# Performance work log

Measured on AMD Instinct MI355X. Metric: run time of the kernel, lower is better.

## Reference

```python
import jax, jax.numpy as jnp
import numpy as np

G = 1024      # graphs per batch
NPG = 64      # nodes per graph
M = 512       # undirected edges per graph (stored both directions)
N = G * NPG   # 65536 nodes
E = G * 2 * M # 1048576 directed edges
F_IN = 128
HID = 128
CLS = 10
RATIO = 0.5   # top-k edge ratio (forward arg `ratio`); eval phase (train_phase=False)


def setup_inputs() -> dict:
    rng = np.random.default_rng(0)
    # random undirected edges within each graph, i < j guaranteed
    a = rng.integers(0, NPG, (G, M))
    b = rng.integers(0, NPG - 1, (G, M))
    b = b + (b >= a)  # b != a
    i = np.minimum(a, b)
    j = np.maximum(a, b)
    off = (np.arange(G) * NPG)[:, None]
    src = (np.concatenate([i, j], axis=1) + off).reshape(-1).astype(np.int32)
    dst = (np.concatenate([j, i], axis=1) + off).reshape(-1).astype(np.int32)
    # reverse-edge pairing: within each graph block of 2M edges, fwd e <-> e+M
    rev = (np.concatenate([np.arange(M) + M, np.arange(M)])[None, :]
           + (np.arange(G) * 2 * M)[:, None]).reshape(-1).astype(np.int32)
    batch = np.repeat(np.arange(G), NPG).astype(np.int32)

    key = jax.random.key(0)
    ks = jax.random.split(key, 8)

    def lin(k, fi, fo):
        return jax.random.normal(k, (fi, fo), jnp.float32) / np.sqrt(fi).astype(np.float32)

    return dict(
        x=jax.random.normal(ks[0], (N, F_IN), jnp.float32),
        src=jnp.asarray(src), dst=jnp.asarray(dst), rev=jnp.asarray(rev),
        batch=jnp.asarray(batch),
        W0=lin(ks[1], F_IN, HID), b0=jnp.zeros((HID,), jnp.float32),
        W1=lin(ks[2], HID, HID), b1=jnp.zeros((HID,), jnp.float32),
        W2=lin(ks[3], HID, HID), b2=jnp.zeros((HID,), jnp.float32),
        lw1=lin(ks[4], HID, HID), lb1=jnp.zeros((HID,), jnp.float32),
        lw2=lin(ks[5], HID, CLS), lb2=jnp.zeros((CLS,), jnp.float32),
    )


def gcn_conv(x, W, b, src, dst, ew):
    # PyG GCNConv with self-loops (fill 1) and symmetric normalization
    h = x @ W                                      # [N,H]
    deg = jax.ops.segment_sum(ew, dst, num_segments=N) + 1.0
    dinv = jax.lax.rsqrt(deg)                      # deg >= 1 (relu'd x => ew >= 0)
    norm = dinv[src] * ew * dinv[dst]              # [E]
    agg = jax.ops.segment_sum(norm[:, None] * h[src], dst, num_segments=N)
    return agg + (dinv * dinv)[:, None] * h + b    # self-loop term + bias


def reference(x, src, dst, rev, batch, W0, b0, W1, b1, W2, b2, lw1, lb1, lw2, lb2):
    ones_e = jnp.ones((E,), x.dtype)
    x1 = jax.nn.relu(gcn_conv(x, W0, b0, src, dst, ones_e))

    # edge scores on relu'd features (nonnegative)
    scores = jnp.sum(x1[src] * x1[dst], axis=-1)   # [E]
    gid = batch[src]                               # per-edge graph id (nondecreasing)
    mask = src < dst                               # one direction per undirected edge

    # per-graph (segment) top-k over masked edges: rank within segment by score desc
    smask = jnp.where(mask, scores, -jnp.inf)
    perm = jnp.lexsort((-smask, gid))              # primary: gid, secondary: score desc
    counts = jax.ops.segment_sum(jnp.ones((E,), jnp.int32), gid, num_segments=G)
    start = jnp.cumsum(counts) - counts            # exclusive segment starts
    rank = jnp.zeros((E,), jnp.int32).at[perm].set(
        jnp.arange(E, dtype=jnp.int32) - start[gid[perm]])
    m = jax.ops.segment_sum(mask.astype(jnp.int32), gid, num_segments=G)
    k = jnp.ceil(RATIO * m.astype(jnp.float32)).astype(jnp.int32)
    sel = mask & (rank < k[gid])
    sampled = (sel | sel[rev]).astype(x.dtype)     # mirror to reverse direction

    ew = scores * sampled                          # sparse edge weights
    x2 = jax.nn.relu(gcn_conv(x1, W1, b1, src, dst, ew))
    x3 = jax.nn.relu(gcn_conv(x2, W2, b2, src, dst, ew))

    # global mean pool over nodes per graph
    nc = jax.ops.segment_sum(jnp.ones((N,), x.dtype), batch, num_segments=G)
    pooled = jax.ops.segment_sum(x3, batch, num_segments=G) / nc[:, None]

    h = jax.nn.relu(pooled @ lw1 + lb1)            # dropout is identity at eval
    logits = h @ lw2 + lb2
    return (jax.nn.log_softmax(logits, axis=-1), sampled, counts)
```

## Files before the change

### kernel.cpp

```cpp
#include <hip/hip_runtime.h>

#define G_   1024
#define NPG_ 64
#define EPG_ 1024
#define MPG_ 512
#define F_   128
#define E_   (G_*EPG_)

typedef __attribute__((ext_vector_type(8))) short bf16x8;
typedef __attribute__((ext_vector_type(4))) float f32x4;

__device__ __forceinline__ unsigned short f2bf(float f) {
    union { float f; unsigned int u; } v; v.f = f;
    unsigned int r = v.u + 0x7fffu + ((v.u >> 16) & 1u);
    return (unsigned short)(r >> 16);
}
__device__ __forceinline__ unsigned int packbf(float a, float b) {
    return (unsigned int)f2bf(a) | ((unsigned int)f2bf(b) << 16);
}

#define XASW(r, cb) ((((r) << 4) + ((cb) ^ ((r) & 15))) << 3)
#define AFSW(r, b)  ((((r) << 3) + ((b) ^ ((r) & 7))) << 3)

__global__ __launch_bounds__(256) void k_pack_w(const float* __restrict__ W0,
    const float* __restrict__ W1, const float* __restrict__ W2,
    unsigned short* __restrict__ Wp)
{
    int idx = blockIdx.x * 256 + threadIdx.x;
    int wsel = idx >> 11;
    int r = idx & 2047;
    int lane = r & 63, tc = (r >> 6) & 7, kb = r >> 9;
    const float* W = (wsel == 0) ? W0 : ((wsel == 1) ? W1 : W2);
    int col  = tc * 16 + (lane & 15);
    int row0 = kb * 32 + (lane >> 4) * 8;
    unsigned int p0 = packbf(W[(row0+0)*F_+col], W[(row0+1)*F_+col]);
    unsigned int p1 = packbf(W[(row0+2)*F_+col], W[(row0+3)*F_+col]);
    unsigned int p2 = packbf(W[(row0+4)*F_+col], W[(row0+5)*F_+col]);
    unsigned int p3 = packbf(W[(row0+6)*F_+col], W[(row0+7)*F_+col]);
    *(uint4*)(Wp + (size_t)wsel * 16384 + (size_t)r * 8) = make_uint4(p0,p1,p2,p3);
}

__global__ __launch_bounds__(256, 4) void k_fused(
    const float* __restrict__ x, const int* __restrict__ src, const int* __restrict__ dst,
    const unsigned short* __restrict__ Wp,
    const float* __restrict__ b0, const float* __restrict__ b1, const float* __restrict__ b2,
    const float* __restrict__ lw1, const float* __restrict__ lb1,
    const float* __restrict__ lw2, const float* __restrict__ lb2,
    float* __restrict__ out_log, float* __restrict__ out_sampled,
    float* __restrict__ out_counts)
{
    const int g = blockIdx.x, t = threadIdx.x;
    const int l = t & 63, w = t >> 6;
    const int q = l >> 4, cl = l & 15;
    const int base_e = g * EPG_, base_n = g * NPG_;

    __shared__ alignas(16) unsigned short XA[8192];
    __shared__ alignas(16) float buf1[4224];
    __shared__ alignas(16) float sc[MPG_];
    __shared__ unsigned char sl[EPG_], dl[EPG_];
    __shared__ int hist_i[256];
    __shared__ unsigned long long mlist[96];
    __shared__ int wsum[4];
    __shared__ float redzf[8];
    __shared__ int ideg[NPG_];
    __shared__ float dinv[NPG_];
    __shared__ int mcnt, bstar, Rrem;

    float* mtmp = (float*)hist_i;
    unsigned int*   a1p = (unsigned int*)buf1;
    unsigned short* af1 = (unsigned short*)buf1 + 4224;
    unsigned short* af2 = (unsigned short*)buf1;

    auto mfma_step1 = [&](const unsigned short* WpX, f32x4 (&cX)[4][2]) {
        #pragma unroll
        for (int rb = 0; rb < 4; rb++) { cX[rb][0] = (f32x4)0.0f; cX[rb][1] = (f32x4)0.0f; }
        #pragma unroll
        for (int kb = 0; kb < 4; kb++) {
            bf16x8 a[4];
            #pragma unroll
            for (int rb = 0; rb < 4; rb++)
                a[rb] = *(const bf16x8*)&XA[XASW(rb*16 + cl, kb*4 + q)];
            #pragma unroll
            for (int tcw = 0; tcw < 2; tcw++) {
                bf16x8 b = *(const bf16x8*)&WpX[((kb*8 + 2*w+tcw)*64 + l)*8];
                #pragma unroll
                for (int rb = 0; rb < 4; rb++)
                    cX[rb][tcw] = __builtin_amdgcn_mfma_f32_16x16x32_bf16(
                                      a[rb], b, cX[rb][tcw], 0, 0, 0);
            }
        }
    };
    auto write_xw = [&](const f32x4 (&cX)[4][2]) {
        #pragma unroll
        for (int rb = 0; rb < 4; rb++)
            #pragma unroll
            for (int tcw = 0; tcw < 2; tcw++) {
                int tc = 2*w + tcw;
                #pragma unroll
                for (int rp = 0; rp < 2; rp++) {
                    int r0 = rb*16 + q*4 + rp*2;
                    int idx = ((r0 >> 5)*8 + tc)*512 + (((r0 >> 3) & 3)*16 + cl)*8 + (r0 & 7);
                    *(unsigned int*)&XA[idx] = packbf(cX[rb][tcw][rp*2], cX[rb][tcw][rp*2+1]);
                }
            }
    };
    auto mfma_step2 = [&](const unsigned short* AFp, f32x4 (&cX)[4][2]) {
        #pragma unroll
        for (int rb = 0; rb < 4; rb++) { cX[rb][0] = (f32x4)0.0f; cX[rb][1] = (f32x4)0.0f; }
        #pragma unroll
        for (int kb2 = 0; kb2 < 2; kb2++) {
            bf16x8 a2[4];
            #pragma unroll
            for (int rb = 0; rb < 4; rb++)
                a2[rb] = *(const bf16x8*)&AFp[AFSW(rb*16 + cl, kb2*4 + q)];
            #pragma unroll
            for (int tcw = 0; tcw < 2; tcw++) {
                bf16x8 b2 = *(const bf16x8*)&XA[((kb2*8 + 2*w+tcw)*64 + l)*8];
                #pragma unroll
                for (int rb = 0; rb < 4; rb++)
                    cX[rb][tcw] = __builtin_amdgcn_mfma_f32_16x16x32_bf16(
                                      a2[rb], b2, cX[rb][tcw], 0, 0, 0);
            }
        }
    };
    auto epilogue_H = [&](const f32x4 (&cX)[4][2], const float* bias) {
        #pragma unroll
        for (int tcw = 0; tcw < 2; tcw++) {
            int colb = (2*w + tcw)*16 + cl;
            float bv = bias[colb];
            #pragma unroll
            for (int rb = 0; rb < 4; rb++)
                #pragma unroll
                for (int reg = 0; reg < 4; reg++) {
                    int row = rb*16 + q*4 + reg;
                    XA[XASW(row, colb >> 3) + (colb & 7)] =
                        f2bf(fmaxf(cX[rb][tcw][reg] + bv, 0.0f));
                }
        }
    };

    const float4* xsrc = (const float4*)(x + (size_t)base_n * F_);
    for (int i = t; i < 2048; i += 256) {
        int v = i >> 5, c4 = i & 31;
        float4 xv = xsrc[i];
        int si = XASW(v, c4 >> 1) + (c4 & 1) * 4;
        unsigned int* d2 = (unsigned int*)&XA[si];
        d2[0] = packbf(xv.x, xv.y);
        d2[1] = packbf(xv.z, xv.w);
    }
    for (int i = t; i < 2112; i += 256) a1p[i] = 0u;
    if (t < NPG_) ideg[t] = 0;
    __syncthreads();

    {
        int4 s4 = ((const int4*)(src + base_e))[t];
        int4 d4 = ((const int4*)(dst + base_e))[t];
        int s0 = s4.x - base_n, s1 = s4.y - base_n, s2 = s4.z - base_n, s3 = s4.w - base_n;
        int d0 = d4.x - base_n, d1 = d4.y - base_n, d2 = d4.z - base_n, d3 = d4.w - base_n;
        *(uchar4*)&sl[t*4] = make_uchar4((unsigned char)s0, (unsigned char)s1,
                                         (unsigned char)s2, (unsigned char)s3);
        *(uchar4*)&dl[t*4] = make_uchar4((unsigned char)d0, (unsigned char)d1,
                                         (unsigned char)d2, (unsigned char)d3);
        atomicAdd(&ideg[d0], 1); atomicAdd(&ideg[d1], 1);
        atomicAdd(&ideg[d2], 1); atomicAdd(&ideg[d3], 1);
        atomicAdd(&a1p[d0 * 33 + (s0 >> 1)], 1u << ((s0 & 1) * 16));
        atomicAdd(&a1p[d1 * 33 + (s1 >> 1)], 1u << ((s1 & 1) * 16));
        atomicAdd(&a1p[d2 * 33 + (s2 >> 1)], 1u << ((s2 & 1) * 16));
        atomicAdd(&a1p[d3 * 33 + (s3 >> 1)], 1u << ((s3 & 1) * 16));
    }
    __syncthreads();

    {
        f32x4 cA[4][2];
        mfma_step1(Wp, cA);
        for (int i = t; i < 4096; i += 256) {
            int v = i >> 6, s = i & 63;
            unsigned int m = (a1p[v * 33 + (s >> 1)] >> ((s & 1) * 16)) & 0xFFFFu;
            float fv = rsqrtf((float)(ideg[v] + 1)), fs = rsqrtf((float)(ideg[s] + 1));
            float a = fv * fs * (float)m;
            if (v == s) a += fv * fv;
            af1[AFSW(v, s >> 3) + (s & 7)] = f2bf(a);
        }
        __syncthreads();
        write_xw(cA);
    }
    __syncthreads();

    {
        f32x4 cB[4][2];
        mfma_step2(af1, cB);
        __syncthreads();
        epilogue_H(cB, b0);
    }
    __syncthreads();

    {
        f32x4 cg[4];
        #pragma unroll
        for (int tcg = 0; tcg < 4; tcg++) cg[tcg] = (f32x4)0.0f;
        #pragma unroll
        for (int kb = 0; kb < 4; kb++) {
            bf16x8 a_g = *(const bf16x8*)&XA[XASW(w*16 + cl, kb*4 + q)];
            #pragma unroll
            for (int tcg = 0; tcg < 4; tcg++) {
                bf16x8 b = *(const bf16x8*)&XA[XASW(tcg*16 + cl, kb*4 + q)];
                cg[tcg] = __builtin_amdgcn_mfma_f32_16x16x32_bf16(a_g, b, cg[tcg], 0, 0, 0);
            }
        }
        #pragma unroll
        for (int tcg = 0; tcg < 4; tcg++)
            #pragma unroll
            for (int reg = 0; reg < 4; reg++)
                buf1[(w*16 + q*4 + reg)*66 + tcg*16 + cl] = cg[tcg][reg];
    }
    __syncthreads();

    float sA, sB;
    {
        f32x4 cC[4][2];
        mfma_step1(Wp + 16384, cC);
        sA = buf1[(int)sl[t]*66 + dl[t]];
        sB = buf1[(int)sl[t+256]*66 + dl[t+256]];
        sc[t] = sA; sc[t + 256] = sB;
        __syncthreads();
        write_xw(cC);
    }
    if (t < NPG_) dinv[t] = 1.0f;
    {
        float mn = fminf(sA, sB), mx = fmaxf(sA, sB);
        #pragma unroll
        for (int off = 32; off >= 1; off >>= 1) {
            mn = fminf(mn, __shfl_xor(mn, off, 64));
            mx = fmaxf(mx, __shfl_xor(mx, off, 64));
        }
        if (l == 0) { redzf[w] = mn; redzf[4 + w] = mx; }
    }
    hist_i[t] = 0;
    if (t == 0) mcnt = 0;
    __syncthreads();

    int selA, selB;
    {
        float mn = fminf(fminf(redzf[0], redzf[1]), fminf(redzf[2], redzf[3]));
        float mx = fmaxf(fmaxf(redzf[4], redzf[5]), fmaxf(redzf[6], redzf[7]));
        float scale = 255.0f / fmaxf(mx - mn, 1e-20f);
        int binA = (int)fminf((sA - mn) * scale, 255.0f);
        int binB = (int)fminf((sB - mn) * scale, 255.0f);
        atomicAdd(&hist_i[binA], 1);
        atomicAdd(&hist_i[binB], 1);
        for (int i = t; i < 4224; i += 256) buf1[i] = 0.0f;
        __syncthreads();
        int h = hist_i[t];
        int v = h;
        #pragma unroll
        for (int off = 1; off < 64; off <<= 1) {
            int n = __shfl_down(v, off, 64);
            if (l + off < 64) v += n;
        }
        if (l == 0) wsum[w] = v;
        __syncthreads();
        int suf = v;
        for (int w2 = w + 1; w2 < 4; w2++) suf += wsum[w2];
        int cgt = suf - h;
        if (suf >= 256 && cgt < 256) { bstar = t; Rrem = 256 - cgt; }
        __syncthreads();
        const int bs = bstar, Rr = Rrem;
        unsigned long long keyA = ((unsigned long long)__float_as_uint(sA) << 32)
                                | (unsigned int)(0xFFFFFFFFu - (unsigned)t);
        unsigned long long keyB = ((unsigned long long)__float_as_uint(sB) << 32)
                                | (unsigned int)(0xFFFFFFFFu - (unsigned)(t + 256));
        if (binA == bs) { int p = atomicAdd(&mcnt, 1); if (p < 96) mlist[p] = keyA; }
        if (binB == bs) { int p = atomicAdd(&mcnt, 1); if (p < 96) mlist[p] = keyB; }
        __syncthreads();
        const int mc = mcnt;
        auto sel_edge = [&](float s, int e, int bin, unsigned long long key) -> int {
            if (bin > bs) return 1;
            if (bin < bs) return 0;
            if (mc <= 96) {
                int r = 0;
                for (int j2 = 0; j2 < mc; j2++) r += (mlist[j2] > key) ? 1 : 0;
                return r < Rr;
            }
            int r = 0;
            for (int ep = 0; ep < MPG_; ep++) {
                float sp = sc[ep];
                r += (sp > s || (sp == s && ep < e)) ? 1 : 0;
            }
            return r < 256;
        };
        selA = sel_edge(sA, t, binA, keyA);
        selB = sel_edge(sB, t + 256, binB, keyB);
        float sfA = selA ? 1.0f : 0.0f, sfB = selB ? 1.0f : 0.0f;
        out_sampled[base_e + t] = sfA;
        out_sampled[base_e + MPG_ + t] = sfA;
        out_sampled[base_e + t + 256] = sfB;
        out_sampled[base_e + MPG_ + t + 256] = sfB;
    }
    if (selA) {
        atomicAdd(&dinv[dl[t]], sA); atomicAdd(&dinv[sl[t]], sA);
        atomicAdd(&buf1[(int)dl[t]*66 + sl[t]], sA);
        atomicAdd(&buf1[(int)sl[t]*66 + dl[t]], sA);
    }
    if (selB) {
        atomicAdd(&dinv[dl[t+256]], sB); atomicAdd(&dinv[sl[t+256]], sB);
        atomicAdd(&buf1[(int)dl[t+256]*66 + sl[t+256]], sB);
        atomicAdd(&buf1[(int)sl[t+256]*66 + dl[t+256]], sB);
    }
    __syncthreads();
    if (t < NPG_) dinv[t] = rsqrtf(dinv[t]);
    if (t < F_)  sc[t] = 0.0f;
    __syncthreads();
    {
        float st[4];
        #pragma unroll
        for (int k2 = 0; k2 < 4; k2++) {
            int i = k2*256 + t; int vv = i >> 6, ss = i & 63;
            float a = dinv[vv] * dinv[ss] * buf1[vv*66 + ss];
            if (vv == ss) a += dinv[vv] * dinv[vv];
            st[k2] = a;
        }
        __syncthreads();
        #pragma unroll
        for (int k2 = 0; k2 < 4; k2++) {
            int i = k2*256 + t; int vv = i >> 6, ss = i & 63;
            af2[AFSW(vv, ss >> 3) + (ss & 7)] = f2bf(st[k2]);
        }
        for (int i = 1024 + t; i < 4096; i += 256) {
            int vv = i >> 6, ss = i & 63;
            float a = dinv[vv] * dinv[ss] * buf1[vv*66 + ss];
            if (vv == ss) a += dinv[vv] * dinv[vv];
            af2[AFSW(vv, ss >> 3) + (ss & 7)] = f2bf(a);
        }
    }
    __syncthreads();

    {
        f32x4 cB[4][2];
        mfma_step2(af2, cB);
        __syncthreads();
        epilogue_H(cB, b1);
    }
    __syncthreads();

    {
        f32x4 cA[4][2];
        mfma_step1(Wp + 32768, cA);
        __syncthreads();
        write_xw(cA);
        __syncthreads();
        f32x4 cB[4][2];
        mfma_step2(af2, cB);
        __syncthreads();
        #pragma unroll
        for (int tcw = 0; tcw < 2; tcw++) {
            int colb = (2*w + tcw)*16 + cl;
            float bv = b2[colb];
            float ps = 0.0f;
            #pragma unroll
            for (int rb = 0; rb < 4; rb++)
                #pragma unroll
                for (int reg = 0; reg < 4; reg++)
                    ps += fmaxf(cB[rb][tcw][reg] + bv, 0.0f);
            atomicAdd(&sc[colb], ps);
        }
    }
    __syncthreads();

    {
        int c = t & 127, hh = t >> 7;
        float p = 0.0f;
        for (int kk = 0; kk < 64; kk++) {
            int k2 = hh*64 + kk;
            p = fmaf(sc[k2], lw1[(size_t)k2 * F_ + c], p);
        }
        mtmp[t] = p;
    }
    __syncthreads();
    if (t >= 128 && t < 138) buf1[200 + (t - 128)] = 0.0f;
    if (t < F_)
        buf1[t] = fmaxf(lb1[t] + (mtmp[t] + mtmp[t + 128]) * (1.0f/64.0f), 0.0f);
    __syncthreads();
    if (t < 160) {
        int o = t >> 4, seg = t & 15;
        float p = 0.0f;
        #pragma unroll
        for (int kk = 0; kk < 8; kk++) {
            int k2 = seg*8 + kk;
            p = fmaf(buf1[k2], lw2[(size_t)k2 * 10 + o], p);
        }
        atomicAdd(&buf1[200 + o], p);
    }
    __syncthreads();
    if (t < 10) {
        float lg = buf1[200 + t] + lb2[t];
        float m = -1e30f;
        #pragma unroll
        for (int q2 = 0; q2 < 10; q2++) m = fmaxf(m, buf1[200 + q2] + lb2[q2]);
        float se = 0.0f;
        #pragma unroll
        for (int q2 = 0; q2 < 10; q2++) se += expf(buf1[200 + q2] + lb2[q2] - m);
        out_log[(size_t)g * 10 + t] = lg - m - logf(se);
    }
    if (t == 0) out_counts[g] = 1024.0f;
}

extern "C" void kernel_launch(void* const* d_in, const int* in_sizes, int n_in,
                              void* d_out, int out_size, void* d_ws, size_t ws_size,
                              hipStream_t stream) {
    const float* x    = (const float*)d_in[0];
    const int*   src  = (const int*)  d_in[1];
    const int*   dst  = (const int*)  d_in[2];
    const float* W0   = (const float*)d_in[5];
    const float* b0   = (const float*)d_in[6];
    const float* W1   = (const float*)d_in[7];
    const float* b1   = (const float*)d_in[8];
    const float* W2   = (const float*)d_in[9];
    const float* b2   = (const float*)d_in[10];
    const float* lw1  = (const float*)d_in[11];
    const float* lb1  = (const float*)d_in[12];
    const float* lw2  = (const float*)d_in[13];
    const float* lb2  = (const float*)d_in[14];

    float* out_log     = (float*)d_out;
    float* out_sampled = out_log + (size_t)G_ * 10;
    float* out_counts  = out_sampled + (size_t)E_;

    unsigned short* Wp = (unsigned short*)d_ws;

    k_pack_w<<<24, 256, 0, stream>>>(W0, W1, W2, Wp);
    k_fused<<<G_, 256, 0, stream>>>(x, src, dst, Wp, b0, b1, b2,
                                    lw1, lb1, lw2, lb2,
                                    out_log, out_sampled, out_counts);
}
```

Before: 48.34 us.

## Double block size to 512 threads, one column tile per wave

```diff
diff --git a/kernel.cpp b/kernel.cpp
--- a/kernel.cpp
+++ b/kernel.cpp
@@ -40,7 +40,7 @@
     *(uint4*)(Wp + (size_t)wsel * 16384 + (size_t)r * 8) = make_uint4(p0,p1,p2,p3);
 }
 
-__global__ __launch_bounds__(256, 4) void k_fused(
+__global__ __launch_bounds__(512, 8) void k_fused(
     const float* __restrict__ x, const int* __restrict__ src, const int* __restrict__ dst,
     const unsigned short* __restrict__ Wp,
     const float* __restrict__ b0, const float* __restrict__ b1, const float* __restrict__ b2,
@@ -61,86 +61,66 @@
     __shared__ int hist_i[256];
     __shared__ unsigned long long mlist[96];
     __shared__ int wsum[4];
-    __shared__ float redzf[8];
+    __shared__ float redzf[16];
     __shared__ int ideg[NPG_];
     __shared__ float dinv[NPG_];
     __shared__ int mcnt, bstar, Rrem;
 
-    float* mtmp = (float*)hist_i;
     unsigned int*   a1p = (unsigned int*)buf1;
     unsigned short* af1 = (unsigned short*)buf1 + 4224;
     unsigned short* af2 = (unsigned short*)buf1;
 
-    auto mfma_step1 = [&](const unsigned short* WpX, f32x4 (&cX)[4][2]) {
-        #pragma unroll
-        for (int rb = 0; rb < 4; rb++) { cX[rb][0] = (f32x4)0.0f; cX[rb][1] = (f32x4)0.0f; }
+    auto mfma_step1 = [&](const unsigned short* WpX, f32x4 (&cX)[4]) {
+        #pragma unroll
+        for (int rb = 0; rb < 4; rb++) cX[rb] = (f32x4)0.0f;
         #pragma unroll
         for (int kb = 0; kb < 4; kb++) {
-            bf16x8 a[4];
-            #pragma unroll
-            for (int rb = 0; rb < 4; rb++)
-                a[rb] = *(const bf16x8*)&XA[XASW(rb*16 + cl, kb*4 + q)];
-            #pragma unroll
-            for (int tcw = 0; tcw < 2; tcw++) {
-                bf16x8 b = *(const bf16x8*)&WpX[((kb*8 + 2*w+tcw)*64 + l)*8];
-                #pragma unroll
-                for (int rb = 0; rb < 4; rb++)
-                    cX[rb][tcw] = __builtin_amdgcn_mfma_f32_16x16x32_bf16(
-                                      a[rb], b, cX[rb][tcw], 0, 0, 0);
+            bf16x8 b = *(const bf16x8*)&WpX[((kb*8 + w)*64 + l)*8];
+            #pragma unroll
+            for (int rb = 0; rb < 4; rb++) {
+                bf16x8 a = *(const bf16x8*)&XA[XASW(rb*16 + cl, kb*4 + q)];
+                cX[rb] = __builtin_amdgcn_mfma_f32_16x16x32_bf16(a, b, cX[rb], 0, 0, 0);
             }
         }
     };
-    auto write_xw = [&](const f32x4 (&cX)[4][2]) {
+    auto write_xw = [&](const f32x4 (&cX)[4]) {
         #pragma unroll
         for (int rb = 0; rb < 4; rb++)
             #pragma unroll
-            for (int tcw = 0; tcw < 2; tcw++) {
-                int tc = 2*w + tcw;
-                #pragma unroll
-                for (int rp = 0; rp < 2; rp++) {
-                    int r0 = rb*16 + q*4 + rp*2;
-                    int idx = ((r0 >> 5)*8 + tc)*512 + (((r0 >> 3) & 3)*16 + cl)*8 + (r0 & 7);
-                    *(unsigned int*)&XA[idx] = packbf(cX[rb][tcw][rp*2], cX[rb][tcw][rp*2+1]);
-                }
+            for (int rp = 0; rp < 2; rp++) {
+                int r0 = rb*16 + q*4 + rp*2;
+                int idx = ((r0 >> 5)*8 + w)*512 + (((r0 >> 3) & 3)*16 + cl)*8 + (r0 & 7);
+                *(unsigned int*)&XA[idx] = packbf(cX[rb][rp*2], cX[rb][rp*2+1]);
             }
     };
-    auto mfma_step2 = [&](const unsigned short* AFp, f32x4 (&cX)[4][2]) {
-        #pragma unroll
-        for (int rb = 0; rb < 4; rb++) { cX[rb][0] = (f32x4)0.0f; cX[rb][1] = (f32x4)0.0f; }
+    auto mfma_step2 = [&](const unsigned short* AFp, f32x4 (&cX)[4]) {
+        #pragma unroll
+        for (int rb = 0; rb < 4; rb++) cX[rb] = (f32x4)0.0f;
         #pragma unroll
         for (int kb2 = 0; kb2 < 2; kb2++) {
-            bf16x8 a2[4];
-            #pragma unroll
-            for (int rb = 0; rb < 4; rb++)
-                a2[rb] = *(const bf16x8*)&AFp[AFSW(rb*16 + cl, kb2*4 + q)];
-            #pragma unroll
-            for (int tcw = 0; tcw < 2; tcw++) {
-                bf16x8 b2 = *(const bf16x8*)&XA[((kb2*8 + 2*w+tcw)*64 + l)*8];
-                #pragma unroll
-                for (int rb = 0; rb < 4; rb++)
-                    cX[rb][tcw] = __builtin_amdgcn_mfma_f32_16x16x32_bf16(
-                                      a2[rb], b2, cX[rb][tcw], 0, 0, 0);
+            bf16x8 b2 = *(const bf16x8*)&XA[((kb2*8 + w)*64 + l)*8];
+            #pragma unroll
+            for (int rb = 0; rb < 4; rb++) {
+                bf16x8 a2 = *(const bf16x8*)&AFp[AFSW(rb*16 + cl, kb2*4 + q)];
+                cX[rb] = __builtin_amdgcn_mfma_f32_16x16x32_bf16(a2, b2, cX[rb], 0, 0, 0);
             }
         }
     };
-    auto epilogue_H = [&](const f32x4 (&cX)[4][2], const float* bias) {
-        #pragma unroll
-        for (int tcw = 0; tcw < 2; tcw++) {
-            int colb = (2*w + tcw)*16 + cl;
-            float bv = bias[colb];
-            #pragma unroll
-            for (int rb = 0; rb < 4; rb++)
-                #pragma unroll
-                for (int reg = 0; reg < 4; reg++) {
-                    int row = rb*16 + q*4 + reg;
-                    XA[XASW(row, colb >> 3) + (colb & 7)] =
-                        f2bf(fmaxf(cX[rb][tcw][reg] + bv, 0.0f));
-                }
-        }
+    auto epilogue_H = [&](const f32x4 (&cX)[4], const float* bias) {
+        int colb = w*16 + cl;
+        float bv = bias[colb];
+        #pragma unroll
+        for (int rb = 0; rb < 4; rb++)
+            #pragma unroll
+            for (int reg = 0; reg < 4; reg++) {
+                int row = rb*16 + q*4 + reg;
+                XA[XASW(row, colb >> 3) + (colb & 7)] =
+                    f2bf(fmaxf(cX[rb][reg] + bv, 0.0f));
+            }
     };
 
     const float4* xsrc = (const float4*)(x + (size_t)base_n * F_);
-    for (int i = t; i < 2048; i += 256) {
+    for (int i = t; i < 2048; i += 512) {
         int v = i >> 5, c4 = i & 31;
         float4 xv = xsrc[i];
         int si = XASW(v, c4 >> 1) + (c4 & 1) * 4;
@@ -148,32 +128,27 @@
         d2[0] = packbf(xv.x, xv.y);
         d2[1] = packbf(xv.z, xv.w);
     }
-    for (int i = t; i < 2112; i += 256) a1p[i] = 0u;
+    for (int i = t; i < 2112; i += 512) a1p[i] = 0u;
     if (t < NPG_) ideg[t] = 0;
     __syncthreads();
 
     {
-        int4 s4 = ((const int4*)(src + base_e))[t];
-        int4 d4 = ((const int4*)(dst + base_e))[t];
-        int s0 = s4.x - base_n, s1 = s4.y - base_n, s2 = s4.z - base_n, s3 = s4.w - base_n;
-        int d0 = d4.x - base_n, d1 = d4.y - base_n, d2 = d4.z - base_n, d3 = d4.w - base_n;
-        *(uchar4*)&sl[t*4] = make_uchar4((unsigned char)s0, (unsigned char)s1,
-                                         (unsigned char)s2, (unsigned char)s3);
-        *(uchar4*)&dl[t*4] = make_uchar4((unsigned char)d0, (unsigned char)d1,
-                                         (unsigned char)d2, (unsigned char)d3);
+        int2 s2 = ((const int2*)(src + base_e))[t];
+        int2 d2 = ((const int2*)(dst + base_e))[t];
+        int s0 = s2.x - base_n, s1 = s2.y - base_n;
+        int d0 = d2.x - base_n, d1 = d2.y - base_n;
+        sl[t*2]   = (unsigned char)s0; sl[t*2+1] = (unsigned char)s1;
+        dl[t*2]   = (unsigned char)d0; dl[t*2+1] = (unsigned char)d1;
         atomicAdd(&ideg[d0], 1); atomicAdd(&ideg[d1], 1);
-        atomicAdd(&ideg[d2], 1); atomicAdd(&ideg[d3], 1);
         atomicAdd(&a1p[d0 * 33 + (s0 >> 1)], 1u << ((s0 & 1) * 16));
         atomicAdd(&a1p[d1 * 33 + (s1 >> 1)], 1u << ((s1 & 1) * 16));
-        atomicAdd(&a1p[d2 * 33 + (s2 >> 1)], 1u << ((s2 & 1) * 16));
-        atomicAdd(&a1p[d3 * 33 + (s3 >> 1)], 1u << ((s3 & 1) * 16));
-    }
-    __syncthreads();
-
-    {
-        f32x4 cA[4][2];
+    }
+    __syncthreads();
+
+    {
+        f32x4 cA[4];
         mfma_step1(Wp, cA);
-        for (int i = t; i < 4096; i += 256) {
+        for (int i = t; i < 4096; i += 512) {
             int v = i >> 6, s = i & 63;
             unsigned int m = (a1p[v * 33 + (s >> 1)] >> ((s & 1) * 16)) & 0xFFFFu;
             float fv = rsqrtf((float)(ideg[v] + 1)), fs = rsqrtf((float)(ideg[s] + 1));
@@ -187,7 +162,7 @@
     __syncthreads();
 
     {
-        f32x4 cB[4][2];
+        f32x4 cB[4];
         mfma_step2(af1, cB);
         __syncthreads();
         epilogue_H(cB, b0);
@@ -195,147 +170,131 @@
     __syncthreads();
 
     {
-        f32x4 cg[4];
-        #pragma unroll
-        for (int tcg = 0; tcg < 4; tcg++) cg[tcg] = (f32x4)0.0f;
+        const int rt = w & 3, ct0 = (w >> 2) * 2;
+        f32x4 cg[2];
+        cg[0] = (f32x4)0.0f; cg[1] = (f32x4)0.0f;
         #pragma unroll
         for (int kb = 0; kb < 4; kb++) {
-            bf16x8 a_g = *(const bf16x8*)&XA[XASW(w*16 + cl, kb*4 + q)];
-            #pragma unroll
-            for (int tcg = 0; tcg < 4; tcg++) {
-                bf16x8 b = *(const bf16x8*)&XA[XASW(tcg*16 + cl, kb*4 + q)];
-                cg[tcg] = __builtin_amdgcn_mfma_f32_16x16x32_bf16(a_g, b, cg[tcg], 0, 0, 0);
-            }
-        }
-        #pragma unroll
-        for (int tcg = 0; tcg < 4; tcg++)
+            bf16x8 a_g = *(const bf16x8*)&XA[XASW(rt*16 + cl, kb*4 + q)];
+            #pragma unroll
+            for (int j = 0; j < 2; j++) {
+                bf16x8 b = *(const bf16x8*)&XA[XASW((ct0+j)*16 + cl, kb*4 + q)];
+                cg[j] = __builtin_amdgcn_mfma_f32_16x16x32_bf16(a_g, b, cg[j], 0, 0, 0);
+            }
+        }
+        #pragma unroll
+        for (int j = 0; j < 2; j++)
             #pragma unroll
             for (int reg = 0; reg < 4; reg++)
-                buf1[(w*16 + q*4 + reg)*66 + tcg*16 + cl] = cg[tcg][reg];
-    }
-    __syncthreads();
-
-    float sA, sB;
-    {
-        f32x4 cC[4][2];
+                buf1[(rt*16 + q*4 + reg)*66 + (ct0+j)*16 + cl] = cg[j][reg];
+    }
+    __syncthreads();
+
+    float sA;
+    {
+        f32x4 cC[4];
         mfma_step1(Wp + 16384, cC);
         sA = buf1[(int)sl[t]*66 + dl[t]];
-        sB = buf1[(int)sl[t+256]*66 + dl[t+256]];
-        sc[t] = sA; sc[t + 256] = sB;
+        sc[t] = sA;
         __syncthreads();
         write_xw(cC);
     }
     if (t < NPG_) dinv[t] = 1.0f;
     {
-        float mn = fminf(sA, sB), mx = fmaxf(sA, sB);
+        float mn = sA, mx = sA;
         #pragma unroll
         for (int off = 32; off >= 1; off >>= 1) {
             mn = fminf(mn, __shfl_xor(mn, off, 64));
             mx = fmaxf(mx, __shfl_xor(mx, off, 64));
         }
-        if (l == 0) { redzf[w] = mn; redzf[4 + w] = mx; }
-    }
-    hist_i[t] = 0;
+        if (l == 0) { redzf[w] = mn; redzf[8 + w] = mx; }
+    }
+    if (t < 256) hist_i[t] = 0;
     if (t == 0) mcnt = 0;
     __syncthreads();
 
-    int selA, selB;
-    {
-        float mn = fminf(fminf(redzf[0], redzf[1]), fminf(redzf[2], redzf[3]));
-        float mx = fmaxf(fmaxf(redzf[4], redzf[5]), fmaxf(redzf[6], redzf[7]));
+    int selA;
+    {
+        float mn = redzf[0], mx = redzf[8];
+        #pragma unroll
+        for (int j = 1; j < 8; j++) { mn = fminf(mn, redzf[j]); mx = fmaxf(mx, redzf[8+j]); }
         float scale = 255.0f / fmaxf(mx - mn, 1e-20f);
         int binA = (int)fminf((sA - mn) * scale, 255.0f);
-        int binB = (int)fminf((sB - mn) * scale, 255.0f);
         atomicAdd(&hist_i[binA], 1);
-        atomicAdd(&hist_i[binB], 1);
-        for (int i = t; i < 4224; i += 256) buf1[i] = 0.0f;
-        __syncthreads();
-        int h = hist_i[t];
-        int v = h;
-        #pragma unroll
-        for (int off = 1; off < 64; off <<= 1) {
-            int n = __shfl_down(v, off, 64);
-            if (l + off < 64) v += n;
-        }
-        if (l == 0) wsum[w] = v;
-        __syncthreads();
-        int suf = v;
-        for (int w2 = w + 1; w2 < 4; w2++) suf += wsum[w2];
-        int cgt = suf - h;
-        if (suf >= 256 && cgt < 256) { bstar = t; Rrem = 256 - cgt; }
+        for (int i = t; i < 4224; i += 512) buf1[i] = 0.0f;
+        __syncthreads();
+        int h = 0, v = 0;
+        if (t < 256) {
+            h = hist_i[t];
+            v = h;
+            #pragma unroll
+            for (int off = 1; off < 64; off <<= 1) {
+                int n = __shfl_down(v, off, 64);
+                if (l + off < 64) v += n;
+            }
+            if (l == 0) wsum[w] = v;
+        }
+        __syncthreads();
+        if (t < 256) {
+            int suf = v;
+            for (int w2 = w + 1; w2 < 4; w2++) suf += wsum[w2];
+            int cgt = suf - h;
+            if (suf >= 256 && cgt < 256) { bstar = t; Rrem = 256 - cgt; }
+        }
         __syncthreads();
         const int bs = bstar, Rr = Rrem;
         unsigned long long keyA = ((unsigned long long)__float_as_uint(sA) << 32)
                                 | (unsigned int)(0xFFFFFFFFu - (unsigned)t);
-        unsigned long long keyB = ((unsigned long long)__float_as_uint(sB) << 32)
-                                | (unsigned int)(0xFFFFFFFFu - (unsigned)(t + 256));
         if (binA == bs) { int p = atomicAdd(&mcnt, 1); if (p < 96) mlist[p] = keyA; }
-        if (binB == bs) { int p = atomicAdd(&mcnt, 1); if (p < 96) mlist[p] = keyB; }
         __syncthreads();
         const int mc = mcnt;
-        auto sel_edge = [&](float s, int e, int bin, unsigned long long key) -> int {
-            if (bin > bs) return 1;
-            if (bin < bs) return 0;
-            if (mc <= 96) {
-                int r = 0;
-                for (int j2 = 0; j2 < mc; j2++) r += (mlist[j2] > key) ? 1 : 0;
-                return r < Rr;
-            }
+        if (binA > bs) selA = 1;
+        else if (binA < bs) selA = 0;
+        else if (mc <= 96) {
+            int r = 0;
+            for (int j2 = 0; j2 < mc; j2++) r += (mlist[j2] > keyA) ? 1 : 0;
+            selA = r < Rr;
+        } else {
             int r = 0;
             for (int ep = 0; ep < MPG_; ep++) {
                 float sp = sc[ep];
-                r += (sp > s || (sp == s && ep < e)) ? 1 : 0;
-            }
-            return r < 256;
-        };
-        selA = sel_edge(sA, t, binA, keyA);
-        selB = sel_edge(sB, t + 256, binB, keyB);
-        float sfA = selA ? 1.0f : 0.0f, sfB = selB ? 1.0f : 0.0f;
+                r += (sp > sA || (sp == sA && ep < t)) ? 1 : 0;
+            }
+            selA = r < 256;
+        }
+        float sfA = selA ? 1.0f : 0.0f;
         out_sampled[base_e + t] = sfA;
         out_sampled[base_e + MPG_ + t] = sfA;
-        out_sampled[base_e + t + 256] = sfB;
-        out_sampled[base_e + MPG_ + t + 256] = sfB;
     }
     if (selA) {
         atomicAdd(&dinv[dl[t]], sA); atomicAdd(&dinv[sl[t]], sA);
         atomicAdd(&buf1[(int)dl[t]*66 + sl[t]], sA);
         atomicAdd(&buf1[(int)sl[t]*66 + dl[t]], sA);
     }
-    if (selB) {
-        atomicAdd(&dinv[dl[t+256]], sB); atomicAdd(&dinv[sl[t+256]], sB);
-        atomicAdd(&buf1[(int)dl[t+256]*66 + sl[t+256]], sB);
-        atomicAdd(&buf1[(int)sl[t+256]*66 + dl[t+256]], sB);
-    }
     __syncthreads();
     if (t < NPG_) dinv[t] = rsqrtf(dinv[t]);
     if (t < F_)  sc[t] = 0.0f;
     __syncthreads();
     {
-        float st[4];
-        #pragma unroll
-        for (int k2 = 0; k2 < 4; k2++) {
-            int i = k2*256 + t; int vv = i >> 6, ss = i & 63;
+        float st[8];
+        #pragma unroll
+        for (int k2 = 0; k2 < 8; k2++) {
+            int i = k2*512 + t; int vv = i >> 6, ss = i & 63;
             float a = dinv[vv] * dinv[ss] * buf1[vv*66 + ss];
             if (vv == ss) a += dinv[vv] * dinv[vv];
             st[k2] = a;
         }
         __syncthreads();
         #pragma unroll
-        for (int k2 = 0; k2 < 4; k2++) {
-            int i = k2*256 + t; int vv = i >> 6, ss = i & 63;
+        for (int k2 = 0; k2 < 8; k2++) {
+            int i = k2*512 + t; int vv = i >> 6, ss = i & 63;
             af2[AFSW(vv, ss >> 3) + (ss & 7)] = f2bf(st[k2]);
         }
-        for (int i = 1024 + t; i < 4096; i += 256) {
-            int vv = i >> 6, ss = i & 63;
-            float a = dinv[vv] * dinv[ss] * buf1[vv*66 + ss];
-            if (vv == ss) a += dinv[vv] * dinv[vv];
-            af2[AFSW(vv, ss >> 3) + (ss & 7)] = f2bf(a);
-        }
-    }
-    __syncthreads();
-
-    {
-        f32x4 cB[4][2];
+    }
+    __syncthreads();
+
+    {
+        f32x4 cB[4];
         mfma_step2(af2, cB);
         __syncthreads();
         epilogue_H(cB, b1);
@@ -343,42 +302,40 @@
     __syncthreads();
 
     {
-        f32x4 cA[4][2];
+        f32x4 cA[4];
         mfma_step1(Wp + 32768, cA);
         __syncthreads();
         write_xw(cA);
         __syncthreads();
-        f32x4 cB[4][2];
+        f32x4 cB[4];
         mfma_step2(af2, cB);
         __syncthreads();
-        #pragma unroll
-        for (int tcw = 0; tcw < 2; tcw++) {
-            int colb = (2*w + tcw)*16 + cl;
-            float bv = b2[colb];
-            float ps = 0.0f;
-            #pragma unroll
-            for (int rb = 0; rb < 4; rb++)
-                #pragma unroll
-                for (int reg = 0; reg < 4; reg++)
-                    ps += fmaxf(cB[rb][tcw][reg] + bv, 0.0f);
-            atomicAdd(&sc[colb], ps);
-        }
+        int colb = w*16 + cl;
+        float bv = b2[colb];
+        float ps = 0.0f;
+        #pragma unroll
+        for (int rb = 0; rb < 4; rb++)
+            #pragma unroll
+            for (int reg = 0; reg < 4; reg++)
+                ps += fmaxf(cB[rb][reg] + bv, 0.0f);
+        atomicAdd(&sc[colb], ps);
+        if (t < 10) buf1[700 + t] = 0.0f;
     }
     __syncthreads();
 
     {
         int c = t & 127, hh = t >> 7;
         float p = 0.0f;
-        for (int kk = 0; kk < 64; kk++) {
-            int k2 = hh*64 + kk;
+        for (int kk = 0; kk < 32; kk++) {
+            int k2 = hh*32 + kk;
             p = fmaf(sc[k2], lw1[(size_t)k2 * F_ + c], p);
         }
-        mtmp[t] = p;
-    }
-    __syncthreads();
-    if (t >= 128 && t < 138) buf1[200 + (t - 128)] = 0.0f;
+        buf1[hh * 128 + c] = p;
+    }
+    __syncthreads();
     if (t < F_)
-        buf1[t] = fmaxf(lb1[t] + (mtmp[t] + mtmp[t + 128]) * (1.0f/64.0f), 0.0f);
+        buf1[512 + t] = fmaxf(lb1[t] + (buf1[t] + buf1[128+t] + buf1[256+t] + buf1[384+t])
+                                        * (1.0f/64.0f), 0.0f);
     __syncthreads();
     if (t < 160) {
         int o = t >> 4, seg = t & 15;
@@ -386,19 +343,19 @@
         #pragma unroll
         for (int kk = 0; kk < 8; kk++) {
             int k2 = seg*8 + kk;
-            p = fmaf(buf1[k2], lw2[(size_t)k2 * 10 + o], p);
-        }
-        atomicAdd(&buf1[200 + o], p);
+            p = fmaf(buf1[512 + k2], lw2[(size_t)k2 * 10 + o], p);
+        }
+        atomicAdd(&buf1[700 + o], p);
     }
     __syncthreads();
     if (t < 10) {
-        float lg = buf1[200 + t] + lb2[t];
+        float lg = buf1[700 + t] + lb2[t];
         float m = -1e30f;
         #pragma unroll
-        for (int q2 = 0; q2 < 10; q2++) m = fmaxf(m, buf1[200 + q2] + lb2[q2]);
+        for (int q2 = 0; q2 < 10; q2++) m = fmaxf(m, buf1[700 + q2] + lb2[q2]);
         float se = 0.0f;
         #pragma unroll
-        for (int q2 = 0; q2 < 10; q2++) se += expf(buf1[200 + q2] + lb2[q2] - m);
+        for (int q2 = 0; q2 < 10; q2++) se += expf(buf1[700 + q2] + lb2[q2] - m);
         out_log[(size_t)g * 10 + t] = lg - m - logf(se);
     }
     if (t == 0) out_counts[g] = 1024.0f;
@@ -428,7 +385,7 @@
     unsigned short* Wp = (unsigned short*)d_ws;
 
     k_pack_w<<<24, 256, 0, stream>>>(W0, W1, W2, Wp);
-    k_fused<<<G_, 256, 0, stream>>>(x, src, dst, Wp, b0, b1, b2,
+    k_fused<<<G_, 512, 0, stream>>>(x, src, dst, Wp, b0, b1, b2,
                                     lw1, lb1, lw2, lb2,
                                     out_log, out_sampled, out_counts);
 }
```

Result: slower. 58.67 us (+21.4%).
